# Performance work log

Hardware: AMD Instinct MI355X
Metric: run time of the kernel (lower is better)

The kernel has to match this reference:

```python
import jax, jax.numpy as jnp
import numpy as np

D_MODEL = 1024
N_HEADS = 16
D_K = D_MODEL // N_HEADS
THETA = 10000.0
B, S = 4, 2048


def setup_inputs() -> dict:
    key = jax.random.key(0)
    ks = jax.random.split(key, 5)
    scale = 0.02
    return {
        "x": jax.random.normal(ks[0], (B, S, D_MODEL), dtype=jnp.float32),
        "token_positions": jnp.arange(S, dtype=jnp.int32),
        "WQ": jax.random.normal(ks[1], (D_MODEL, D_MODEL), dtype=jnp.float32) * scale,
        "WK": jax.random.normal(ks[2], (D_MODEL, D_MODEL), dtype=jnp.float32) * scale,
        "WV": jax.random.normal(ks[3], (D_MODEL, D_MODEL), dtype=jnp.float32) * scale,
        "WO": jax.random.normal(ks[4], (D_MODEL, D_MODEL), dtype=jnp.float32) * scale,
    }


def apply_rope(x, positions):
    # x: [B, H, S, d_k]; rotate interleaved (even, odd) pairs
    half = D_K // 2
    inv_freq = THETA ** (-jnp.arange(half, dtype=x.dtype) * 2.0 / D_K)  # [half]
    ang = positions.astype(x.dtype)[:, None] * inv_freq[None, :]        # [S, half]
    cos, sin = jnp.cos(ang), jnp.sin(ang)
    x1 = x[..., 0::2]
    x2 = x[..., 1::2]
    r1 = x1 * cos - x2 * sin
    r2 = x1 * sin + x2 * cos
    return jnp.stack([r1, r2], axis=-1).reshape(x.shape)


def reference(x, token_positions, WQ, WK, WV, WO):
    b, s, _ = x.shape
    # Linear (no bias), weight stored (out, in): y = x @ W^T
    def proj(W):
        y = jnp.einsum('bsd,ed->bse', x, W)
        return y.reshape(b, s, N_HEADS, D_K).transpose(0, 2, 1, 3)  # [b,h,s,dk]
    Q, K, V = proj(WQ), proj(WK), proj(WV)
    Q = apply_rope(Q, token_positions)
    K = apply_rope(K, token_positions)
    scores = jnp.einsum('bhqd,bhkd->bhqk', Q, K) / jnp.sqrt(jnp.asarray(D_K, x.dtype))
    causal = jnp.tril(jnp.ones((s, s), dtype=bool))
    scores = jnp.where(causal, scores, -jnp.inf)
    attn = jax.nn.softmax(scores, axis=-1)
    out = jnp.einsum('bhqk,bhkd->bhqd', attn, V)
    out = out.transpose(0, 2, 1, 3).reshape(b, s, D_MODEL)
    return jnp.einsum('bse,de->bsd', out, WO)
```

## Files before the change

### kernel.cpp

```cpp
#include <hip/hip_runtime.h>
#include <cstdint>
#include <cstddef>

#define DM 1024
#define NH 16
#define DKD 64
#define BB 4
#define SS 2048
#define MTOT (BB*SS)

typedef float  f32x4  __attribute__((ext_vector_type(4)));
typedef __bf16 bf16x8 __attribute__((ext_vector_type(8)));
typedef __bf16 bf16x4v __attribute__((ext_vector_type(4)));
typedef __bf16 bf16x2v __attribute__((ext_vector_type(2)));
using as3v = __attribute__((address_space(3))) void;
using as1v = __attribute__((address_space(1))) void;

__device__ __forceinline__ void gl2lds16(const void* g, void* l) {
  __builtin_amdgcn_global_load_lds((as1v*)g, (as3v*)l, 16, 0, 0);
}

__device__ __forceinline__ float fast_exp2(float x) {
#if __has_builtin(__builtin_amdgcn_exp2f)
  return __builtin_amdgcn_exp2f(x);
#else
  return __expf(x * 0.6931471805599453f);
#endif
}

__device__ __forceinline__ void sincos_rev(float rev, float* s, float* c) {
#if __has_builtin(__builtin_amdgcn_sinf) && __has_builtin(__builtin_amdgcn_cosf)
  *s = __builtin_amdgcn_sinf(rev);
  *c = __builtin_amdgcn_cosf(rev);
#else
  float a = rev * 6.283185307179586f;
  *s = __sinf(a); *c = __cosf(a);
#endif
}

__global__ void cast_all_k(const float* __restrict__ x,
                           const float* __restrict__ wq, const float* __restrict__ wk,
                           const float* __restrict__ wv, const float* __restrict__ wo,
                           __bf16* __restrict__ xb,
                           __bf16* __restrict__ wqb, __bf16* __restrict__ wkb,
                           __bf16* __restrict__ wvb, __bf16* __restrict__ wob) {
  int i = blockIdx.x * blockDim.x + threadIdx.x;
  const float* src;
  __bf16* dst;
  int idx, oidx;
  if (i < 2097152) {
    src = x; dst = xb; idx = i; oidx = i;
  } else {
    int j = i - 2097152;
    int w = j >> 18;
    idx = j & 262143;
    src = (w == 0) ? wq : (w == 1) ? wk : (w == 2) ? wv : wo;
    dst = (w == 0) ? wqb : (w == 1) ? wkb : (w == 2) ? wvb : wob;
    if (w < 2) {
      int e = idx >> 8;
      int c = idx & 255;
      int d = e & 63;
      int dp = (d & 1) ? 32 + (d >> 1) : (d >> 1);
      oidx = (((e & ~63) | dp) << 8) | c;
    } else {
      oidx = idx;
    }
  }
  float4 f = ((const float4*)src)[idx];
  bf16x4v o;
  o[0] = (__bf16)f.x; o[1] = (__bf16)f.y; o[2] = (__bf16)f.z; o[3] = (__bf16)f.w;
  ((bf16x4v*)dst)[oidx] = o;
}

__global__ void rope_tbl_k(const int* __restrict__ pos, float2* __restrict__ tbl) {
  int p = blockIdx.x * blockDim.x + threadIdx.x;
  int s = p >> 5;
  int i = p & 31;
  float ps = (float)pos[s];
  float invr = __expf(-0.28782313663f * (float)i) * 0.15915494309f;
  float rev = ps * invr;
  rev -= floorf(rev);
  float sn, cs;
  sincos_rev(rev, &sn, &cs);
  tbl[p] = make_float2(cs, sn);
}

template <typename CT>
__global__ __launch_bounds__(256) void gemm_bt_k(const __bf16* __restrict__ A,
                                                 const __bf16* __restrict__ B,
                                                 CT* __restrict__ C,
                                                 int M, int N, int K) {
  __shared__ __bf16 As[128 * 32];
  __shared__ __bf16 Bs[128 * 32];
  const int tid  = threadIdx.x;
  const int lane = tid & 63;
  const int wid  = tid >> 6;
  const int lrow = lane & 15;
  const int quad = lane >> 4;
  const int m0 = blockIdx.y * 128;
  const int n0 = blockIdx.x * 128;
  const int wm = (wid & 1) * 64;
  const int wn = (wid >> 1) * 64;
  const int srow = wid * 32 + (lane >> 2);
  const int scol = (lane & 3) * 8;

  f32x4 acc[4][4] = {};

  for (int k0 = 0; k0 < K; k0 += 32) {
    __syncthreads();
    gl2lds16(A + (size_t)(m0 + srow)      * K + k0 + scol, As + (wid * 32)      * 32);
    gl2lds16(A + (size_t)(m0 + srow + 16) * K + k0 + scol, As + (wid * 32 + 16) * 32);
    gl2lds16(B + (size_t)(n0 + srow)      * K + k0 + scol, Bs + (wid * 32)      * 32);
    gl2lds16(B + (size_t)(n0 + srow + 16) * K + k0 + scol, Bs + (wid * 32 + 16) * 32);
    __syncthreads();

    bf16x8 af[4], bfr[4];
#pragma unroll
    for (int i = 0; i < 4; ++i)
      af[i] = *(const bf16x8*)(As + (wm + i * 16 + lrow) * 32 + quad * 8);
#pragma unroll
    for (int i = 0; i < 4; ++i)
      bfr[i] = *(const bf16x8*)(Bs + (wn + i * 16 + lrow) * 32 + quad * 8);
#pragma unroll
    for (int mi = 0; mi < 4; ++mi)
#pragma unroll
      for (int ni = 0; ni < 4; ++ni)
        acc[mi][ni] = __builtin_amdgcn_mfma_f32_16x16x32_bf16(af[mi], bfr[ni], acc[mi][ni], 0, 0, 0);
  }

#pragma unroll
  for (int mi = 0; mi < 4; ++mi)
#pragma unroll
    for (int ni = 0; ni < 4; ++ni)
#pragma unroll
      for (int r = 0; r < 4; ++r) {
        int row = m0 + wm + mi * 16 + quad * 4 + r;
        int col = n0 + wn + ni * 16 + lrow;
        C[(size_t)row * N + col] = (CT)acc[mi][ni][r];
      }
}

__global__ __launch_bounds__(256) void gemm_qkv_k(const __bf16* __restrict__ A,
                                                  const __bf16* __restrict__ Bq,
                                                  const __bf16* __restrict__ Bk,
                                                  const __bf16* __restrict__ Bv,
                                                  const float2* __restrict__ tbl,
                                                  __bf16* __restrict__ Cq,
                                                  __bf16* __restrict__ Ck,
                                                  __bf16* __restrict__ Cv) {
  __shared__ __bf16 As[128 * 32];
  __shared__ __bf16 Bs[128 * 32];
  const int sel = blockIdx.x >> 3;
  const __bf16* B = sel == 0 ? Bq : sel == 1 ? Bk : Bv;
  const int n0 = (blockIdx.x & 7) * 128;
  const int m0 = blockIdx.y * 128;
  const int K = DM;
  const int tid  = threadIdx.x;
  const int lane = tid & 63;
  const int wid  = tid >> 6;
  const int lrow = lane & 15;
  const int quad = lane >> 4;
  const int wm = (wid & 1) * 64;
  const int wn = (wid >> 1) * 64;
  const int srow = wid * 32 + (lane >> 2);
  const int scol = (lane & 3) * 8;

  f32x4 acc[4][4] = {};

  for (int k0 = 0; k0 < K; k0 += 32) {
    __syncthreads();
    gl2lds16(A + (size_t)(m0 + srow)      * K + k0 + scol, As + (wid * 32)      * 32);
    gl2lds16(A + (size_t)(m0 + srow + 16) * K + k0 + scol, As + (wid * 32 + 16) * 32);
    gl2lds16(B + (size_t)(n0 + srow)      * K + k0 + scol, Bs + (wid * 32)      * 32);
    gl2lds16(B + (size_t)(n0 + srow + 16) * K + k0 + scol, Bs + (wid * 32 + 16) * 32);
    __syncthreads();

    bf16x8 af[4], bfr[4];
#pragma unroll
    for (int i = 0; i < 4; ++i)
      af[i] = *(const bf16x8*)(As + (wm + i * 16 + lrow) * 32 + quad * 8);
#pragma unroll
    for (int i = 0; i < 4; ++i)
      bfr[i] = *(const bf16x8*)(Bs + (wn + i * 16 + lrow) * 32 + quad * 8);
#pragma unroll
    for (int mi = 0; mi < 4; ++mi)
#pragma unroll
      for (int ni = 0; ni < 4; ++ni)
        acc[mi][ni] = __builtin_amdgcn_mfma_f32_16x16x32_bf16(af[mi], bfr[ni], acc[mi][ni], 0, 0, 0);
  }

  const int hbase = (n0 + wn) >> 6;
  const int bq = m0 >> 11;

  if (sel == 2) {
    __bf16* vt = Cv + ((size_t)(bq * NH + hbase)) * (DKD * SS);
    const int sbase = ((m0 + wm) & (SS - 1)) + quad * 4;
#pragma unroll
    for (int ni = 0; ni < 4; ++ni) {
      const int d = ni * 16 + lrow;
#pragma unroll
      for (int mi = 0; mi < 4; ++mi) {
        bf16x4v pk;
#pragma unroll
        for (int r = 0; r < 4; ++r) pk[r] = (__bf16)acc[mi][ni][r];
        *(bf16x4v*)(vt + (size_t)d * SS + sbase + mi * 16) = pk;
      }
    }
  } else {
    __bf16* C = ((sel == 0) ? Cq : Ck) + ((size_t)(bq * NH + hbase)) * (SS * DKD);
#pragma unroll
    for (int ni = 0; ni < 2; ++ni) {
      const int i = ni * 16 + lrow;
#pragma unroll
      for (int mi = 0; mi < 4; ++mi) {
#pragma unroll
        for (int r = 0; r < 4; ++r) {
          int s = (m0 + wm + mi * 16 + quad * 4 + r) & (SS - 1);
          float2 cssn = tbl[s * 32 + i];
          float a = acc[mi][ni][r];
          float b = acc[mi][ni + 2][r];
          C[(size_t)s * DKD + i]      = (__bf16)fmaf(a, cssn.x, -(b * cssn.y));
          C[(size_t)s * DKD + 32 + i] = (__bf16)fmaf(a, cssn.y,  (b * cssn.x));
        }
      }
    }
  }
}

__global__ __launch_bounds__(512, 4) void attn7_k(const __bf16* __restrict__ Qh,
                                                  const __bf16* __restrict__ Kh,
                                                  const __bf16* __restrict__ VT,
                                                  __bf16* __restrict__ O) {
  __shared__ __bf16 Ks[128 * 64];
  __shared__ __bf16 Vt[64 * 128];
  __shared__ __bf16 Pt[8][16 * 136];
  const int tid  = threadIdx.x;
  const int lane = tid & 63;
  const int wid  = tid >> 6;
  const int lrow = lane & 15;
  const int quad = lane >> 4;
  const int j   = blockIdx.x;
  const int xcd = j & 7;
  const int t   = j >> 3;
  const int bh  = (xcd << 3) | (t >> 4);
  const int u   = t & 15;
  const int qi  = (u & 1) ? (u >> 1) : (15 - (u >> 1));
  const int b  = bh >> 4;
  const int h  = bh & 15;
  const int q0 = qi * 128;
  const size_t hb = (size_t)bh * (SS * DKD);
  const int qg = q0 + wid * 16 + lrow;

  bf16x8 qf0, qf1;
  {
    const __bf16* qp = Qh + hb + (size_t)qg * DKD + quad * 8;
    qf0 = *(const bf16x8*)qp;
    qf1 = *(const bf16x8*)(qp + 32);
  }
  f32x4 Oa[4] = {};
  float l = 0.f;
  const int nkt = qi + 1;

  const int skr = lane >> 3;
  const int skc = lane & 7;
  const int svd = lane >> 4;
  const int svc = lane & 15;

  for (int kt = 0; kt < nkt; ++kt) {
    __syncthreads();
#pragma unroll
    for (int ii = 0; ii < 2; ++ii) {
      int i = wid * 2 + ii;
      int key = i * 8 + skr;
      int gc = skc ^ (key & 7);
      gl2lds16(Kh + hb + (size_t)(kt * 128 + key) * DKD + gc * 8, Ks + i * 512);
      int dk = i * 4 + svd;
      int gc2 = (svc & 8) | ((svc ^ dk) & 7);
      gl2lds16(VT + hb + (size_t)dk * SS + kt * 128 + gc2 * 8, Vt + i * 512);
    }
    __syncthreads();

    f32x4 sa[8];
#pragma unroll
    for (int mi = 0; mi < 8; ++mi) sa[mi] = (f32x4){0.f, 0.f, 0.f, 0.f};
#pragma unroll
    for (int tt = 0; tt < 2; ++tt) {
      bf16x8 qf = tt ? qf1 : qf0;
#pragma unroll
      for (int mi = 0; mi < 8; ++mi) {
        bf16x8 kf = *(const bf16x8*)(Ks + (mi * 16 + lrow) * 64 + (((tt * 4 + quad) ^ (lrow & 7)) * 8));
        sa[mi] = __builtin_amdgcn_mfma_f32_16x16x32_bf16(kf, qf, sa[mi], 0, 0, 0);
      }
    }

    if (kt == nkt - 1) {
#pragma unroll
      for (int mi = 0; mi < 8; ++mi) {
        bf16x4v pk;
#pragma unroll
        for (int r = 0; r < 4; ++r) {
          int key = kt * 128 + mi * 16 + quad * 4 + r;
          float p = fast_exp2(sa[mi][r] * 0.18033688f - 8.0f);
          p = (key <= qg) ? p : 0.f;
          l += p;
          pk[r] = (__bf16)p;
        }
        *(bf16x4v*)(&Pt[wid][lrow * 136 + mi * 16 + quad * 4]) = pk;
      }
    } else {
#pragma unroll
      for (int mi = 0; mi < 8; ++mi) {
        bf16x4v pk;
#pragma unroll
        for (int r = 0; r < 4; ++r) {
          float p = fast_exp2(sa[mi][r] * 0.18033688f - 8.0f);
          l += p;
          pk[r] = (__bf16)p;
        }
        *(bf16x4v*)(&Pt[wid][lrow * 136 + mi * 16 + quad * 4]) = pk;
      }
    }

#pragma unroll
    for (int kc = 0; kc < 4; ++kc) {
      bf16x8 pf = *(const bf16x8*)(&Pt[wid][lrow * 136 + kc * 32 + quad * 8]);
#pragma unroll
      for (int ni = 0; ni < 4; ++ni) {
        int c = kc * 4 + quad;
        int cp = (c & 8) | ((c ^ (lrow & 7)) & 7);
        bf16x8 vf = *(const bf16x8*)(Vt + (ni * 16 + lrow) * 128 + cp * 8);
        Oa[ni] = __builtin_amdgcn_mfma_f32_16x16x32_bf16(pf, vf, Oa[ni], 0, 0, 0);
      }
    }
  }

  l += __shfl_xor(l, 16, 64);
  l += __shfl_xor(l, 32, 64);

#pragma unroll
  for (int r = 0; r < 4; ++r) {
    float li = __shfl(l, quad * 4 + r, 64);
    float inv = 1.0f / li;
    int row = q0 + wid * 16 + quad * 4 + r;
#pragma unroll
    for (int ni = 0; ni < 4; ++ni)
      O[(size_t)b * SS * DM + (size_t)row * DM + h * DKD + ni * 16 + lrow] =
          (__bf16)(Oa[ni][r] * inv);
  }
}

extern "C" void kernel_launch(void* const* d_in, const int* in_sizes, int n_in,
                              void* d_out, int out_size, void* d_ws, size_t ws_size,
                              hipStream_t stream) {
  (void)in_sizes; (void)n_in; (void)out_size; (void)ws_size;
  const float* x  = (const float*)d_in[0];
  const int*   pos = (const int*)d_in[1];
  const float* WQ = (const float*)d_in[2];
  const float* WK = (const float*)d_in[3];
  const float* WV = (const float*)d_in[4];
  const float* WO = (const float*)d_in[5];
  float* out = (float*)d_out;

  char* w = (char*)d_ws;
  const size_t MB = 1024 * 1024;
  __bf16* xb  = (__bf16*)(w);
  __bf16* wqb = (__bf16*)(w + 16 * MB);
  __bf16* wkb = (__bf16*)(w + 18 * MB);
  __bf16* wvb = (__bf16*)(w + 20 * MB);
  __bf16* wob = (__bf16*)(w + 22 * MB);
  __bf16* Qh  = (__bf16*)(w + 24 * MB);
  __bf16* Kh  = (__bf16*)(w + 40 * MB);
  __bf16* Cb  = (__bf16*)(w + 56 * MB);
  __bf16* VT  = (__bf16*)(w + 72 * MB);
  float2* tbl = (float2*)(w + 88 * MB);

  cast_all_k<<<3145728 / 256, 256, 0, stream>>>(x, WQ, WK, WV, WO, xb, wqb, wkb, wvb, wob);

  rope_tbl_k<<<(SS * 32) / 256, 256, 0, stream>>>(pos, tbl);

  gemm_qkv_k<<<dim3(24, MTOT / 128), 256, 0, stream>>>(xb, wqb, wkb, wvb, tbl, Qh, Kh, VT);

  attn7_k<<<dim3(1024), 512, 0, stream>>>(Qh, Kh, VT, Cb);

  gemm_bt_k<float><<<dim3(DM / 128, MTOT / 128), 256, 0, stream>>>(Cb, wob, out, MTOT, DM, DM);
}
```

Baseline: 286.7 us.

## Double-buffer K/V tiles and keep softmax probabilities in registers via permlane swaps

The attention kernel now prefetches the next K/V tile into a second LDS buffer while the current tile is computed, which drops one barrier per iteration. The probability matrix is no longer written to and read back from LDS. It is packed into bf16 pairs and rearranged across lanes with v_permlane32/16_swap so it can feed the PV MFMA directly. s_setprio is raised around the MFMA sections. This hides global-load latency and cuts LDS traffic. The cost is doubled K/V LDS footprint and a lane-permutation layout that must exactly match the MFMA operand layout.

```diff
diff --git a/kernel.cpp b/kernel.cpp
--- a/kernel.cpp
+++ b/kernel.cpp
@@ -36,6 +36,19 @@
   float a = rev * 6.283185307179586f;
   *s = __sinf(a); *c = __cosf(a);
 #endif
+}
+
+__device__ __forceinline__ uint32_t pkbf(float a, float b) {
+  union { uint32_t u; __bf16 h[2]; } c;
+  c.h[0] = (__bf16)a; c.h[1] = (__bf16)b;
+  return c.u;
+}
+
+__device__ __forceinline__ void permlane32_swap(uint32_t& a, uint32_t& b) {
+  asm volatile("v_permlane32_swap_b32 %0, %1" : "+v"(a), "+v"(b));
+}
+__device__ __forceinline__ void permlane16_swap(uint32_t& a, uint32_t& b) {
+  asm volatile("v_permlane16_swap_b32 %0, %1" : "+v"(a), "+v"(b));
 }
 
 __global__ void cast_all_k(const float* __restrict__ x,
@@ -227,13 +240,12 @@
   }
 }
 
-__global__ __launch_bounds__(512, 4) void attn7_k(const __bf16* __restrict__ Qh,
+__global__ __launch_bounds__(512, 4) void attn8_k(const __bf16* __restrict__ Qh,
                                                   const __bf16* __restrict__ Kh,
                                                   const __bf16* __restrict__ VT,
                                                   __bf16* __restrict__ O) {
-  __shared__ __bf16 Ks[128 * 64];
-  __shared__ __bf16 Vt[64 * 128];
-  __shared__ __bf16 Pt[8][16 * 136];
+  __shared__ __bf16 Ks[2][128 * 64];
+  __shared__ __bf16 Vt[2][64 * 128];
   const int tid  = threadIdx.x;
   const int lane = tid & 63;
   const int wid  = tid >> 6;
@@ -266,71 +278,85 @@
   const int svd = lane >> 4;
   const int svc = lane & 15;
 
-  for (int kt = 0; kt < nkt; ++kt) {
-    __syncthreads();
+  auto stage = [&](int kt, int bsel) {
 #pragma unroll
     for (int ii = 0; ii < 2; ++ii) {
       int i = wid * 2 + ii;
       int key = i * 8 + skr;
       int gc = skc ^ (key & 7);
-      gl2lds16(Kh + hb + (size_t)(kt * 128 + key) * DKD + gc * 8, Ks + i * 512);
+      gl2lds16(Kh + hb + (size_t)(kt * 128 + key) * DKD + gc * 8, &Ks[bsel][i * 512]);
       int dk = i * 4 + svd;
       int gc2 = (svc & 8) | ((svc ^ dk) & 7);
-      gl2lds16(VT + hb + (size_t)dk * SS + kt * 128 + gc2 * 8, Vt + i * 512);
-    }
+      gl2lds16(VT + hb + (size_t)dk * SS + kt * 128 + gc2 * 8, &Vt[bsel][i * 512]);
+    }
+  };
+
+  stage(0, 0);
+
+  for (int kt = 0; kt < nkt; ++kt) {
     __syncthreads();
+    if (kt + 1 < nkt) stage(kt + 1, (kt + 1) & 1);
+    const __bf16* ks = Ks[kt & 1];
+    const __bf16* vt = Vt[kt & 1];
 
     f32x4 sa[8];
 #pragma unroll
     for (int mi = 0; mi < 8; ++mi) sa[mi] = (f32x4){0.f, 0.f, 0.f, 0.f};
+    __builtin_amdgcn_s_setprio(1);
 #pragma unroll
     for (int tt = 0; tt < 2; ++tt) {
       bf16x8 qf = tt ? qf1 : qf0;
 #pragma unroll
       for (int mi = 0; mi < 8; ++mi) {
-        bf16x8 kf = *(const bf16x8*)(Ks + (mi * 16 + lrow) * 64 + (((tt * 4 + quad) ^ (lrow & 7)) * 8));
+        bf16x8 kf = *(const bf16x8*)(ks + (mi * 16 + lrow) * 64 + (((tt * 4 + quad) ^ (lrow & 7)) * 8));
         sa[mi] = __builtin_amdgcn_mfma_f32_16x16x32_bf16(kf, qf, sa[mi], 0, 0, 0);
       }
     }
+    __builtin_amdgcn_s_setprio(0);
 
     if (kt == nkt - 1) {
 #pragma unroll
-      for (int mi = 0; mi < 8; ++mi) {
-        bf16x4v pk;
+      for (int mi = 0; mi < 8; ++mi)
 #pragma unroll
         for (int r = 0; r < 4; ++r) {
           int key = kt * 128 + mi * 16 + quad * 4 + r;
           float p = fast_exp2(sa[mi][r] * 0.18033688f - 8.0f);
           p = (key <= qg) ? p : 0.f;
           l += p;
-          pk[r] = (__bf16)p;
+          sa[mi][r] = p;
         }
-        *(bf16x4v*)(&Pt[wid][lrow * 136 + mi * 16 + quad * 4]) = pk;
-      }
     } else {
 #pragma unroll
-      for (int mi = 0; mi < 8; ++mi) {
-        bf16x4v pk;
+      for (int mi = 0; mi < 8; ++mi)
 #pragma unroll
         for (int r = 0; r < 4; ++r) {
           float p = fast_exp2(sa[mi][r] * 0.18033688f - 8.0f);
           l += p;
-          pk[r] = (__bf16)p;
+          sa[mi][r] = p;
         }
-        *(bf16x4v*)(&Pt[wid][lrow * 136 + mi * 16 + quad * 4]) = pk;
-      }
     }
 
 #pragma unroll
     for (int kc = 0; kc < 4; ++kc) {
-      bf16x8 pf = *(const bf16x8*)(&Pt[wid][lrow * 136 + kc * 32 + quad * 8]);
+      uint32_t w0 = pkbf(sa[kc * 2][0],     sa[kc * 2][1]);
+      uint32_t w1 = pkbf(sa[kc * 2][2],     sa[kc * 2][3]);
+      uint32_t w2 = pkbf(sa[kc * 2 + 1][0], sa[kc * 2 + 1][1]);
+      uint32_t w3 = pkbf(sa[kc * 2 + 1][2], sa[kc * 2 + 1][3]);
+      permlane32_swap(w0, w2);
+      permlane16_swap(w0, w2);
+      permlane32_swap(w1, w3);
+      permlane16_swap(w1, w3);
+      union { uint32_t u[4]; bf16x8 v; } P;
+      P.u[0] = w0; P.u[1] = w1; P.u[2] = w2; P.u[3] = w3;
+      __builtin_amdgcn_s_setprio(1);
 #pragma unroll
       for (int ni = 0; ni < 4; ++ni) {
         int c = kc * 4 + quad;
         int cp = (c & 8) | ((c ^ (lrow & 7)) & 7);
-        bf16x8 vf = *(const bf16x8*)(Vt + (ni * 16 + lrow) * 128 + cp * 8);
-        Oa[ni] = __builtin_amdgcn_mfma_f32_16x16x32_bf16(pf, vf, Oa[ni], 0, 0, 0);
+        bf16x8 vf = *(const bf16x8*)(vt + (ni * 16 + lrow) * 128 + cp * 8);
+        Oa[ni] = __builtin_amdgcn_mfma_f32_16x16x32_bf16(P.v, vf, Oa[ni], 0, 0, 0);
       }
+      __builtin_amdgcn_s_setprio(0);
     }
   }
 
@@ -380,7 +406,7 @@
 
   gemm_qkv_k<<<dim3(24, MTOT / 128), 256, 0, stream>>>(xb, wqb, wkb, wvb, tbl, Qh, Kh, VT);
 
-  attn7_k<<<dim3(1024), 512, 0, stream>>>(Qh, Kh, VT, Cb);
+  attn8_k<<<dim3(1024), 512, 0, stream>>>(Qh, Kh, VT, Cb);
 
   gemm_bt_k<float><<<dim3(DM / 128, MTOT / 128), 256, 0, stream>>>(Cb, wob, out, MTOT, DM, DM);
 }
```

Result: slower. 294.3 us (+2.6%).
